# Kernel tuning notes

Measured on AMD Instinct MI355X. Metric: run time of the kernel, lower is better.

The kernel has to match this reference:

```python
import jax, jax.numpy as jnp
import numpy as np

GROUP = 16  # quantization group size along in_features
EPS = 1e-5


def setup_inputs() -> dict:
    key = jax.random.key(0)
    ks = jax.random.split(key, 6)
    B, D, L, R = 16384, 1024, 18, 32
    x = jax.random.normal(ks[0], (B, D), dtype=jnp.float32)
    # 4-bit codes in [0,16); shifted by -8 at dequant time -> values in [-8,7]
    wq = jax.random.randint(ks[1], (L, D, D), 0, 16, dtype=jnp.int32)
    # per-group positive scales, small so dequantized weights are O(0.1)
    scales = jax.random.uniform(ks[2], (L, D, D // GROUP), dtype=jnp.float32) * 0.05 + 0.005
    bias = jax.random.normal(ks[3], (L, D), dtype=jnp.float32) * 0.02
    # LoRA weights are zero-init in the module; use small random values so the
    # low-rank path is numerically exercised
    lora_a = jax.random.normal(ks[4], (L, R, D), dtype=jnp.float32) * 0.02
    lora_b = jax.random.normal(ks[5], (L, D, R), dtype=jnp.float32) * 0.02
    ln_gamma = jnp.ones((5, D), dtype=jnp.float32)
    ln_beta = jnp.zeros((5, D), dtype=jnp.float32)
    return {"x": x, "wq": wq, "scales": scales, "bias": bias,
            "lora_a": lora_a, "lora_b": lora_b,
            "ln_gamma": ln_gamma, "ln_beta": ln_beta}


def _dequant(wq_i, sc_i):
    # wq_i: [out, in] int codes; sc_i: [out, in//GROUP]
    O, I = wq_i.shape
    q = wq_i.astype(jnp.float32) - 8.0
    w = q.reshape(O, I // GROUP, GROUP) * sc_i[:, :, None]
    return w.reshape(O, I)


def _qlora(x, wq_i, sc_i, b_i, a_i, bm_i):
    w = _dequant(wq_i, sc_i)                       # [out, in]
    base = x @ w.T + b_i                           # frozen 4-bit base path
    lora = (x @ a_i.T) @ bm_i.T                    # low-rank adapter path
    return base + lora


def _layernorm(x, g, b):
    m = jnp.mean(x, axis=-1, keepdims=True)
    v = jnp.mean(jnp.square(x - m), axis=-1, keepdims=True)
    return (x - m) * jax.lax.rsqrt(v + EPS) * g + b


def reference(x, wq, scales, bias, lora_a, lora_b, ln_gamma, ln_beta):
    h = x
    for j in range(6):  # 6 residual blocks, 3 QLoRA layers each
        i = 3 * j
        r = h
        h = jax.nn.relu(_qlora(h, wq[i], scales[i], bias[i], lora_a[i], lora_b[i]))
        h = jax.nn.relu(_qlora(h, wq[i + 1], scales[i + 1], bias[i + 1], lora_a[i + 1], lora_b[i + 1]))
        h = _qlora(h, wq[i + 2], scales[i + 2], bias[i + 2], lora_a[i + 2], lora_b[i + 2])
        h = h + r
        if j < 5:
            h = _layernorm(h, ln_gamma[j], ln_beta[j])
    return h
```

## Files before the change

kernel.cpp:

```cpp
#include <hip/hip_runtime.h>
#include <hip/hip_bf16.h>
#include <stdint.h>

using bf16 = __hip_bfloat16;
typedef __attribute__((ext_vector_type(8))) short bf16x8;
typedef __attribute__((ext_vector_type(8))) unsigned short u16x8;
typedef __attribute__((ext_vector_type(4))) float f32x4;

#define B_ROWS 16384
#define D_DIM  1024
#define NLAYER 18

__device__ inline void gload_lds16(const bf16* g, bf16* l) {
    __builtin_amdgcn_global_load_lds(
        (const __attribute__((address_space(1))) void*)g,
        (__attribute__((address_space(3))) void*)l, 16, 0, 0);
}

__device__ inline unsigned short f2bf_bits(float f) {
    bf16 h = __float2bfloat16(f);
    return *reinterpret_cast<unsigned short*>(&h);
}
__device__ inline float bfbits2f(unsigned short u) {
    unsigned int x = ((unsigned int)u) << 16;
    return __uint_as_float(x);
}
__device__ inline void split_bf(float v, unsigned short& hi, unsigned short& lo) {
    hi = f2bf_bits(v);
    float hf = bfbits2f(hi);
    lo = f2bf_bits(v - hf);
}

__global__ __launch_bounds__(256)
void build_weff(const int* __restrict__ wq, const float* __restrict__ scales,
                const float* __restrict__ lora_a, const float* __restrict__ lora_b,
                bf16* __restrict__ weff_h, bf16* __restrict__ weff_l)
{
    const int bb = blockIdx.x;
    const int l  = bb >> 7;
    const int o0 = (bb & 127) * 8;
    __shared__ float bsh[8][32];
    {
        const int oo = threadIdx.x >> 5, rr = threadIdx.x & 31;
        bsh[oo][rr] = lora_b[((size_t)l * 1024 + o0 + oo) * 32 + rr];
    }
    __syncthreads();

    const float* abase = lora_a + (size_t)l * 32 * 1024;
    const int i0 = threadIdx.x * 4;
    float acc[8][4] = {};
    #pragma unroll 4
    for (int r = 0; r < 32; ++r) {
        float4 av = *reinterpret_cast<const float4*>(abase + (size_t)r * 1024 + i0);
        #pragma unroll
        for (int o = 0; o < 8; ++o) {
            const float br = bsh[o][r];
            acc[o][0] += br * av.x; acc[o][1] += br * av.y;
            acc[o][2] += br * av.z; acc[o][3] += br * av.w;
        }
    }
    #pragma unroll
    for (int o = 0; o < 8; ++o) {
        const size_t row = (size_t)l * 1024 + o0 + o;
        int4 q = *reinterpret_cast<const int4*>(wq + row * 1024 + i0);
        const float sc = scales[row * 64 + (i0 >> 4)];
        float w0 = (q.x - 8) * sc + acc[o][0];
        float w1 = (q.y - 8) * sc + acc[o][1];
        float w2 = (q.z - 8) * sc + acc[o][2];
        float w3 = (q.w - 8) * sc + acc[o][3];
        ushort4 uh, ul;
        split_bf(w0, uh.x, ul.x); split_bf(w1, uh.y, ul.y);
        split_bf(w2, uh.z, ul.z); split_bf(w3, uh.w, ul.w);
        *reinterpret_cast<ushort4*>(weff_h + row * 1024 + i0) = uh;
        *reinterpret_cast<ushort4*>(weff_l + row * 1024 + i0) = ul;
    }
}

__global__ __launch_bounds__(256)
void cast_split(const float* __restrict__ x, bf16* __restrict__ yh, bf16* __restrict__ yl)
{
    size_t i = ((size_t)blockIdx.x * 256 + threadIdx.x) * 4;
    float4 v = *reinterpret_cast<const float4*>(x + i);
    ushort4 uh, ul;
    split_bf(v.x, uh.x, ul.x); split_bf(v.y, uh.y, ul.y);
    split_bf(v.z, uh.z, ul.z); split_bf(v.w, uh.w, ul.w);
    *reinterpret_cast<ushort4*>(yh + i) = uh;
    *reinterpret_cast<ushort4*>(yl + i) = ul;
}

#define TILE_E 8192
#define SET_E  (4 * TILE_E)

#define SCHED0 __builtin_amdgcn_sched_barrier(0)

template<int MODE>
__global__ __launch_bounds__(512)
void qgemm3(const bf16* __restrict__ AH, const bf16* __restrict__ AL,
            const bf16* __restrict__ WH, const bf16* __restrict__ WL,
            const float* __restrict__ bias,
            const bf16* __restrict__ RH, const bf16* __restrict__ RL,
            bf16* __restrict__ OH, bf16* __restrict__ OL,
            float* __restrict__ Of)
{
    __shared__ bf16 smem[2 * SET_E];

    const int b  = blockIdx.x;
    const int sb = ((b & 7) << 5) | (b >> 3);
    const int n0 = (sb & 3) * 256;
    const int m0 = (sb >> 2) * 256;

    const int tid  = threadIdx.x;
    const int wave = tid >> 6;
    const int lane = tid & 63;
    const int wr = wave >> 2;
    const int wc = wave & 3;

    const int rl = lane >> 2;
    const int ps = lane & 3;
    const int fr = lane & 15;
    const int fq = lane >> 4;

    f32x4 acc[8][4] = {};

    auto stage = [&](int buf, int k0) {
        bf16* base = smem + buf * SET_E;
        #pragma unroll
        for (int t = 0; t < 2; ++t) {
            int s = wave * 2 + t;
            int r = s * 16 + rl;
            int q = ps ^ (r & 3) ^ ((r >> 2) & 3);
            size_t ga = (size_t)(m0 + r) * D_DIM + k0 + q * 8;
            size_t gb = (size_t)(n0 + r) * D_DIM + k0 + q * 8;
            bf16* dst = base + s * 512;
            gload_lds16(AH + ga, dst);
            gload_lds16(AL + ga, dst + TILE_E);
            gload_lds16(WH + gb, dst + 2 * TILE_E);
            gload_lds16(WL + gb, dst + 3 * TILE_E);
        }
    };

    stage(0, 0);

    #pragma unroll 1
    for (int kt = 0; kt < 32; ++kt) {
        const int cur = kt & 1;
        SCHED0;
        asm volatile("s_waitcnt vmcnt(0)" ::: "memory");
        SCHED0;
        __builtin_amdgcn_s_barrier();
        if (kt < 31)
            stage(cur ^ 1, (kt + 1) * 32);
        SCHED0;

        const bf16* tb = smem + cur * SET_E;
        bf16x8 wh[4], wl[4], ah[8], al[8];
        #pragma unroll
        for (int n = 0; n < 4; ++n) {
            int R = wc * 64 + n * 16 + fr;
            int p = fq ^ (R & 3) ^ ((R >> 2) & 3);
            int off = R * 32 + p * 8;
            wh[n] = *reinterpret_cast<const bf16x8*>(tb + 2 * TILE_E + off);
            wl[n] = *reinterpret_cast<const bf16x8*>(tb + 3 * TILE_E + off);
        }
        #pragma unroll
        for (int m = 0; m < 8; ++m) {
            int R = wr * 128 + m * 16 + fr;
            int p = fq ^ (R & 3) ^ ((R >> 2) & 3);
            int off = R * 32 + p * 8;
            ah[m] = *reinterpret_cast<const bf16x8*>(tb + off);
            al[m] = *reinterpret_cast<const bf16x8*>(tb + TILE_E + off);
        }

        __builtin_amdgcn_s_setprio(1);
        #pragma unroll
        for (int m = 0; m < 8; ++m)
            #pragma unroll
            for (int n = 0; n < 4; ++n) {
                acc[m][n] = __builtin_amdgcn_mfma_f32_16x16x32_bf16(ah[m], wh[n], acc[m][n], 0, 0, 0);
                acc[m][n] = __builtin_amdgcn_mfma_f32_16x16x32_bf16(ah[m], wl[n], acc[m][n], 0, 0, 0);
                acc[m][n] = __builtin_amdgcn_mfma_f32_16x16x32_bf16(al[m], wh[n], acc[m][n], 0, 0, 0);
            }
        __builtin_amdgcn_s_setprio(0);
    }

    SCHED0;
    asm volatile("s_waitcnt lgkmcnt(0)" ::: "memory");
    SCHED0;
    __builtin_amdgcn_s_barrier();

    const int crow4 = (lane >> 4) * 4;
    float* cwave = reinterpret_cast<float*>(smem) + wave * 4096;
    const int rloc = lane >> 3;
    const int cloc = (lane & 7) * 8;

    #pragma unroll
    for (int half = 0; half < 2; ++half) {
        #pragma unroll
        for (int n = 0; n < 4; ++n) {
            const float bv = bias[n0 + wc * 64 + n * 16 + fr];
            const int lcol = n * 16 + fr;
            const int chunk = lcol >> 2;
            #pragma unroll
            for (int mm = 0; mm < 4; ++mm) {
                const int m = half * 4 + mm;
                #pragma unroll
                for (int j = 0; j < 4; ++j) {
                    const int lrow = mm * 16 + crow4 + j;
                    float v = acc[m][n][j] + bv;
                    if (MODE == 0) v = v > 0.f ? v : 0.f;
                    cwave[lrow * 64 + (chunk ^ (lrow & 15)) * 4 + (lcol & 3)] = v;
                }
            }
        }
        SCHED0;
        asm volatile("s_waitcnt lgkmcnt(0)" ::: "memory");
        SCHED0;

        #pragma unroll
        for (int pass = 0; pass < 8; ++pass) {
            const int lrow = pass * 8 + rloc;
            const int grow = m0 + wr * 128 + half * 64 + lrow;
            const size_t gbase = (size_t)grow * D_DIM + (n0 + wc * 64 + cloc);
            const int c0 = cloc >> 2;
            float4 v0 = *reinterpret_cast<const float4*>(&cwave[lrow * 64 + ((c0    ) ^ (lrow & 15)) * 4]);
            float4 v1 = *reinterpret_cast<const float4*>(&cwave[lrow * 64 + ((c0 + 1) ^ (lrow & 15)) * 4]);
            float vv[8] = {v0.x, v0.y, v0.z, v0.w, v1.x, v1.y, v1.z, v1.w};
            if (MODE != 0) {
                u16x8 rh = *reinterpret_cast<const u16x8*>(&RH[gbase]);
                u16x8 rl2 = *reinterpret_cast<const u16x8*>(&RL[gbase]);
                #pragma unroll
                for (int k = 0; k < 8; ++k)
                    vv[k] += bfbits2f(rh[k]) + bfbits2f(rl2[k]);
            }
            if (MODE == 2) {
                *reinterpret_cast<float4*>(&Of[gbase])     = make_float4(vv[0], vv[1], vv[2], vv[3]);
                *reinterpret_cast<float4*>(&Of[gbase + 4]) = make_float4(vv[4], vv[5], vv[6], vv[7]);
            } else {
                u16x8 ho, lo2;
                #pragma unroll
                for (int k = 0; k < 8; ++k) {
                    unsigned short h, l2;
                    split_bf(vv[k], h, l2);
                    ho[k] = h; lo2[k] = l2;
                }
                *reinterpret_cast<u16x8*>(&OH[gbase]) = ho;
                *reinterpret_cast<u16x8*>(&OL[gbase]) = lo2;
            }
        }
        SCHED0;
        asm volatile("s_waitcnt lgkmcnt(0)" ::: "memory");
        SCHED0;
    }
}

__global__ __launch_bounds__(256)
void ln_pair(const bf16* __restrict__ XH, const bf16* __restrict__ XL,
             bf16* __restrict__ YH, bf16* __restrict__ YL,
             const float* __restrict__ gamma, const float* __restrict__ beta)
{
    const int row = blockIdx.x;
    const int tid = threadIdx.x;
    const int lane = tid & 63;
    const int wave = tid >> 6;

    ushort4 uh = reinterpret_cast<const ushort4*>(XH + (size_t)row * D_DIM)[tid];
    ushort4 ul = reinterpret_cast<const ushort4*>(XL + (size_t)row * D_DIM)[tid];
    float v0 = bfbits2f(uh.x) + bfbits2f(ul.x);
    float v1 = bfbits2f(uh.y) + bfbits2f(ul.y);
    float v2 = bfbits2f(uh.z) + bfbits2f(ul.z);
    float v3 = bfbits2f(uh.w) + bfbits2f(ul.w);
    float s  = v0 + v1 + v2 + v3;
    float ss = v0 * v0 + v1 * v1 + v2 * v2 + v3 * v3;
    #pragma unroll
    for (int off = 32; off >= 1; off >>= 1) {
        s  += __shfl_xor(s, off, 64);
        ss += __shfl_xor(ss, off, 64);
    }
    __shared__ float red[8];
    if (lane == 0) { red[wave] = s; red[4 + wave] = ss; }
    __syncthreads();
    float S  = red[0] + red[1] + red[2] + red[3];
    float SS = red[4] + red[5] + red[6] + red[7];
    const float mean = S * (1.0f / D_DIM);
    const float var  = SS * (1.0f / D_DIM) - mean * mean;
    const float inv  = rsqrtf(var + 1e-5f);

    const int c0 = tid * 4;
    float y0 = (v0 - mean) * inv * gamma[c0 + 0] + beta[c0 + 0];
    float y1 = (v1 - mean) * inv * gamma[c0 + 1] + beta[c0 + 1];
    float y2 = (v2 - mean) * inv * gamma[c0 + 2] + beta[c0 + 2];
    float y3 = (v3 - mean) * inv * gamma[c0 + 3] + beta[c0 + 3];
    ushort4 oh, ol;
    split_bf(y0, oh.x, ol.x); split_bf(y1, oh.y, ol.y);
    split_bf(y2, oh.z, ol.z); split_bf(y3, oh.w, ol.w);
    reinterpret_cast<ushort4*>(YH + (size_t)row * D_DIM)[tid] = oh;
    reinterpret_cast<ushort4*>(YL + (size_t)row * D_DIM)[tid] = ol;
}

extern "C" void kernel_launch(void* const* d_in, const int* in_sizes, int n_in,
                              void* d_out, int out_size, void* d_ws, size_t ws_size,
                              hipStream_t stream)
{
    const float* x      = (const float*)d_in[0];
    const int*   wq     = (const int*)d_in[1];
    const float* scales = (const float*)d_in[2];
    const float* bias   = (const float*)d_in[3];
    const float* lora_a = (const float*)d_in[4];
    const float* lora_b = (const float*)d_in[5];
    const float* ln_g   = (const float*)d_in[6];
    const float* ln_b   = (const float*)d_in[7];
    float* out = (float*)d_out;

    char* ws = (char*)d_ws;
    const size_t W_ELEMS = (size_t)NLAYER * D_DIM * D_DIM;
    const size_t H_ELEMS = (size_t)B_ROWS * D_DIM;
    bf16* WHp = (bf16*)ws;
    bf16* WLp = WHp + W_ELEMS;
    bf16* HAh = WLp + W_ELEMS;
    bf16* HAl = HAh + H_ELEMS;
    bf16* HBh = HAl + H_ELEMS;
    bf16* HBl = HBh + H_ELEMS;
    bf16* HCh = (bf16*)d_out;
    bf16* HCl = HCh + H_ELEMS;

    build_weff<<<dim3(NLAYER * 128), dim3(256), 0, stream>>>(wq, scales, lora_a, lora_b, WHp, WLp);
    cast_split<<<dim3((B_ROWS * D_DIM) / (256 * 4)), dim3(256), 0, stream>>>(x, HAh, HAl);

    dim3 ggrid(256);
    for (int j = 0; j < 6; ++j) {
        const int l0 = 3 * j;
        const bf16* WH0 = WHp + (size_t)l0 * D_DIM * D_DIM;
        const bf16* WL0 = WLp + (size_t)l0 * D_DIM * D_DIM;
        const bf16* WH1 = WHp + (size_t)(l0 + 1) * D_DIM * D_DIM;
        const bf16* WL1 = WLp + (size_t)(l0 + 1) * D_DIM * D_DIM;
        const bf16* WH2 = WHp + (size_t)(l0 + 2) * D_DIM * D_DIM;
        const bf16* WL2 = WLp + (size_t)(l0 + 2) * D_DIM * D_DIM;
        const float* b0 = bias + (size_t)l0 * D_DIM;
        const float* b1 = bias + (size_t)(l0 + 1) * D_DIM;
        const float* b2 = bias + (size_t)(l0 + 2) * D_DIM;
        if (j < 5) {
            qgemm3<0><<<ggrid, 512, 0, stream>>>(HAh, HAl, WH0, WL0, b0, nullptr, nullptr, HBh, HBl, nullptr);
            qgemm3<0><<<ggrid, 512, 0, stream>>>(HBh, HBl, WH1, WL1, b1, nullptr, nullptr, HCh, HCl, nullptr);
            qgemm3<1><<<ggrid, 512, 0, stream>>>(HCh, HCl, WH2, WL2, b2, HAh, HAl, HBh, HBl, nullptr);
            ln_pair<<<dim3(B_ROWS), dim3(256), 0, stream>>>(HBh, HBl, HAh, HAl,
                                                            ln_g + (size_t)j * D_DIM, ln_b + (size_t)j * D_DIM);
        } else {
            qgemm3<0><<<ggrid, 512, 0, stream>>>(HAh, HAl, WH0, WL0, b0, nullptr, nullptr, HCh, HCl, nullptr);
            qgemm3<0><<<ggrid, 512, 0, stream>>>(HCh, HCl, WH1, WL1, b1, nullptr, nullptr, HBh, HBl, nullptr);
            qgemm3<2><<<ggrid, 512, 0, stream>>>(HBh, HBl, WH2, WL2, b2, HAh, HAl, nullptr, nullptr, out);
        }
    }
}
```

Measured before the change: 1.766 ms.

## Shrink GEMM tile to 256x128 and add triple-buffered LDS pipeline

Changes the output tile per block from 256x256 to 256x128, giving 512 blocks instead of 256 so all CUs are covered with better balance. Each wave now owns a 64x64 accumulator tile (half the registers). The LDS staging moves from double to triple buffering with a partial vmcnt wait, keeping two K-steps of loads in flight. The trade-off is lower arithmetic intensity per block, since A tiles are re-read by twice as many blocks, and a larger LDS footprint.

Result: slower. 2.118 ms (+19.9%).

```diff
diff --git a/kernel.cpp b/kernel.cpp
--- a/kernel.cpp
+++ b/kernel.cpp
@@ -88,8 +88,9 @@
     *reinterpret_cast<ushort4*>(yl + i) = ul;
 }
 
-#define TILE_E 8192
-#define SET_E  (4 * TILE_E)
+#define TILE_A 8192
+#define TILE_W 4096
+#define SET_E  (2 * TILE_A + 2 * TILE_W)
 
 #define SCHED0 __builtin_amdgcn_sched_barrier(0)
 
@@ -102,78 +103,81 @@
             bf16* __restrict__ OH, bf16* __restrict__ OL,
             float* __restrict__ Of)
 {
-    __shared__ bf16 smem[2 * SET_E];
+    __shared__ bf16 smem[3 * SET_E];
 
     const int b  = blockIdx.x;
-    const int sb = ((b & 7) << 5) | (b >> 3);
-    const int n0 = (sb & 3) * 256;
-    const int m0 = (sb >> 2) * 256;
+    const int sb = ((b & 7) << 6) | (b >> 3);
+    const int n0 = (sb & 7) * 128;
+    const int m0 = (sb >> 3) * 256;
 
     const int tid  = threadIdx.x;
     const int wave = tid >> 6;
     const int lane = tid & 63;
-    const int wr = wave >> 2;
-    const int wc = wave & 3;
+    const int wr = wave >> 1;
+    const int wc = wave & 1;
 
     const int rl = lane >> 2;
     const int ps = lane & 3;
     const int fr = lane & 15;
     const int fq = lane >> 4;
 
-    f32x4 acc[8][4] = {};
+    f32x4 acc[4][4] = {};
 
     auto stage = [&](int buf, int k0) {
         bf16* base = smem + buf * SET_E;
         #pragma unroll
-        for (int t = 0; t < 2; ++t) {
-            int s = wave * 2 + t;
-            int r = s * 16 + rl;
-            int q = ps ^ (r & 3) ^ ((r >> 2) & 3);
-            size_t ga = (size_t)(m0 + r) * D_DIM + k0 + q * 8;
-            size_t gb = (size_t)(n0 + r) * D_DIM + k0 + q * 8;
-            bf16* dst = base + s * 512;
-            gload_lds16(AH + ga, dst);
-            gload_lds16(AL + ga, dst + TILE_E);
-            gload_lds16(WH + gb, dst + 2 * TILE_E);
-            gload_lds16(WL + gb, dst + 3 * TILE_E);
+        for (int j = 0; j < 6; ++j) {
+            const int c = wave * 6 + j;
+            int seg, tOff, rowBase;
+            const bf16* src;
+            if (c < 16)      { seg = c;      tOff = 0;                   src = AH; rowBase = m0; }
+            else if (c < 32) { seg = c - 16; tOff = TILE_A;              src = AL; rowBase = m0; }
+            else if (c < 40) { seg = c - 32; tOff = 2 * TILE_A;          src = WH; rowBase = n0; }
+            else             { seg = c - 40; tOff = 2 * TILE_A + TILE_W; src = WL; rowBase = n0; }
+            const int r = seg * 16 + rl;
+            const int q = ps ^ (r & 3) ^ ((r >> 2) & 3);
+            gload_lds16(src + (size_t)(rowBase + r) * D_DIM + k0 + q * 8,
+                        base + tOff + seg * 512);
         }
     };
 
     stage(0, 0);
+    stage(1, 32);
 
     #pragma unroll 1
     for (int kt = 0; kt < 32; ++kt) {
-        const int cur = kt & 1;
+        const int cur = kt % 3;
         SCHED0;
-        asm volatile("s_waitcnt vmcnt(0)" ::: "memory");
+        if (kt < 31) asm volatile("s_waitcnt vmcnt(6)" ::: "memory");
+        else         asm volatile("s_waitcnt vmcnt(0)" ::: "memory");
         SCHED0;
         __builtin_amdgcn_s_barrier();
-        if (kt < 31)
-            stage(cur ^ 1, (kt + 1) * 32);
+        if (kt < 30)
+            stage((kt + 2) % 3, (kt + 2) * 32);
         SCHED0;
 
         const bf16* tb = smem + cur * SET_E;
-        bf16x8 wh[4], wl[4], ah[8], al[8];
+        bf16x8 wh[4], wl[4], ah[4], al[4];
         #pragma unroll
         for (int n = 0; n < 4; ++n) {
             int R = wc * 64 + n * 16 + fr;
             int p = fq ^ (R & 3) ^ ((R >> 2) & 3);
             int off = R * 32 + p * 8;
-            wh[n] = *reinterpret_cast<const bf16x8*>(tb + 2 * TILE_E + off);
-            wl[n] = *reinterpret_cast<const bf16x8*>(tb + 3 * TILE_E + off);
-        }
-        #pragma unroll
-        for (int m = 0; m < 8; ++m) {
-            int R = wr * 128 + m * 16 + fr;
+            wh[n] = *reinterpret_cast<const bf16x8*>(tb + 2 * TILE_A + off);
+            wl[n] = *reinterpret_cast<const bf16x8*>(tb + 2 * TILE_A + TILE_W + off);
+        }
+        #pragma unroll
+        for (int m = 0; m < 4; ++m) {
+            int R = wr * 64 + m * 16 + fr;
             int p = fq ^ (R & 3) ^ ((R >> 2) & 3);
             int off = R * 32 + p * 8;
             ah[m] = *reinterpret_cast<const bf16x8*>(tb + off);
-            al[m] = *reinterpret_cast<const bf16x8*>(tb + TILE_E + off);
+            al[m] = *reinterpret_cast<const bf16x8*>(tb + TILE_A + off);
         }
 
         __builtin_amdgcn_s_setprio(1);
         #pragma unroll
-        for (int m = 0; m < 8; ++m)
+        for (int m = 0; m < 4; ++m)
             #pragma unroll
             for (int n = 0; n < 4; ++n) {
                 acc[m][n] = __builtin_amdgcn_mfma_f32_16x16x32_bf16(ah[m], wh[n], acc[m][n], 0, 0, 0);
@@ -194,62 +198,55 @@
     const int cloc = (lane & 7) * 8;
 
     #pragma unroll
-    for (int half = 0; half < 2; ++half) {
-        #pragma unroll
-        for (int n = 0; n < 4; ++n) {
-            const float bv = bias[n0 + wc * 64 + n * 16 + fr];
-            const int lcol = n * 16 + fr;
-            const int chunk = lcol >> 2;
+    for (int n = 0; n < 4; ++n) {
+        const float bv = bias[n0 + wc * 64 + n * 16 + fr];
+        const int lcol = n * 16 + fr;
+        const int chunk = lcol >> 2;
+        #pragma unroll
+        for (int m = 0; m < 4; ++m) {
             #pragma unroll
-            for (int mm = 0; mm < 4; ++mm) {
-                const int m = half * 4 + mm;
-                #pragma unroll
-                for (int j = 0; j < 4; ++j) {
-                    const int lrow = mm * 16 + crow4 + j;
-                    float v = acc[m][n][j] + bv;
-                    if (MODE == 0) v = v > 0.f ? v : 0.f;
-                    cwave[lrow * 64 + (chunk ^ (lrow & 15)) * 4 + (lcol & 3)] = v;
-                }
+            for (int j = 0; j < 4; ++j) {
+                const int lrow = m * 16 + crow4 + j;
+                float v = acc[m][n][j] + bv;
+                if (MODE == 0) v = v > 0.f ? v : 0.f;
+                cwave[lrow * 64 + (chunk ^ (lrow & 15)) * 4 + (lcol & 3)] = v;
             }
         }
-        SCHED0;
-        asm volatile("s_waitcnt lgkmcnt(0)" ::: "memory");
-        SCHED0;
-
-        #pragma unroll
-        for (int pass = 0; pass < 8; ++pass) {
-            const int lrow = pass * 8 + rloc;
-            const int grow = m0 + wr * 128 + half * 64 + lrow;
-            const size_t gbase = (size_t)grow * D_DIM + (n0 + wc * 64 + cloc);
-            const int c0 = cloc >> 2;
-            float4 v0 = *reinterpret_cast<const float4*>(&cwave[lrow * 64 + ((c0    ) ^ (lrow & 15)) * 4]);
-            float4 v1 = *reinterpret_cast<const float4*>(&cwave[lrow * 64 + ((c0 + 1) ^ (lrow & 15)) * 4]);
-            float vv[8] = {v0.x, v0.y, v0.z, v0.w, v1.x, v1.y, v1.z, v1.w};
-            if (MODE != 0) {
-                u16x8 rh = *reinterpret_cast<const u16x8*>(&RH[gbase]);
-                u16x8 rl2 = *reinterpret_cast<const u16x8*>(&RL[gbase]);
-                #pragma unroll
-                for (int k = 0; k < 8; ++k)
-                    vv[k] += bfbits2f(rh[k]) + bfbits2f(rl2[k]);
+    }
+    SCHED0;
+    asm volatile("s_waitcnt lgkmcnt(0)" ::: "memory");
+    SCHED0;
+
+    #pragma unroll
+    for (int pass = 0; pass < 8; ++pass) {
+        const int lrow = pass * 8 + rloc;
+        const int grow = m0 + wr * 64 + lrow;
+        const size_t gbase = (size_t)grow * D_DIM + (n0 + wc * 64 + cloc);
+        const int c0 = cloc >> 2;
+        float4 v0 = *reinterpret_cast<const float4*>(&cwave[lrow * 64 + ((c0    ) ^ (lrow & 15)) * 4]);
+        float4 v1 = *reinterpret_cast<const float4*>(&cwave[lrow * 64 + ((c0 + 1) ^ (lrow & 15)) * 4]);
+        float vv[8] = {v0.x, v0.y, v0.z, v0.w, v1.x, v1.y, v1.z, v1.w};
+        if (MODE != 0) {
+            u16x8 rh = *reinterpret_cast<const u16x8*>(&RH[gbase]);
+            u16x8 rl2 = *reinterpret_cast<const u16x8*>(&RL[gbase]);
+            #pragma unroll
+            for (int k = 0; k < 8; ++k)
+                vv[k] += bfbits2f(rh[k]) + bfbits2f(rl2[k]);
+        }
+        if (MODE == 2) {
+            *reinterpret_cast<float4*>(&Of[gbase])     = make_float4(vv[0], vv[1], vv[2], vv[3]);
+            *reinterpret_cast<float4*>(&Of[gbase + 4]) = make_float4(vv[4], vv[5], vv[6], vv[7]);
+        } else {
+            u16x8 ho, lo2;
+            #pragma unroll
+            for (int k = 0; k < 8; ++k) {
+                unsigned short h, l2;
+                split_bf(vv[k], h, l2);
+                ho[k] = h; lo2[k] = l2;
             }
-            if (MODE == 2) {
-                *reinterpret_cast<float4*>(&Of[gbase])     = make_float4(vv[0], vv[1], vv[2], vv[3]);
-                *reinterpret_cast<float4*>(&Of[gbase + 4]) = make_float4(vv[4], vv[5], vv[6], vv[7]);
-            } else {
-                u16x8 ho, lo2;
-                #pragma unroll
-                for (int k = 0; k < 8; ++k) {
-                    unsigned short h, l2;
-                    split_bf(vv[k], h, l2);
-                    ho[k] = h; lo2[k] = l2;
-                }
-                *reinterpret_cast<u16x8*>(&OH[gbase]) = ho;
-                *reinterpret_cast<u16x8*>(&OL[gbase]) = lo2;
-            }
-        }
-        SCHED0;
-        asm volatile("s_waitcnt lgkmcnt(0)" ::: "memory");
-        SCHED0;
+            *reinterpret_cast<u16x8*>(&OH[gbase]) = ho;
+            *reinterpret_cast<u16x8*>(&OL[gbase]) = lo2;
+        }
     }
 }
 
@@ -326,7 +323,7 @@
     build_weff<<<dim3(NLAYER * 128), dim3(256), 0, stream>>>(wq, scales, lora_a, lora_b, WHp, WLp);
     cast_split<<<dim3((B_ROWS * D_DIM) / (256 * 4)), dim3(256), 0, stream>>>(x, HAh, HAl);
 
-    dim3 ggrid(256);
+    dim3 ggrid(512);
     for (int j = 0; j < 6; ++j) {
         const int l0 = 3 * j;
         const bf16* WH0 = WHp + (size_t)l0 * D_DIM * D_DIM;
```
